# Optimization experiments

Hardware: AMD Instinct MI355X
Metric: run time of the kernel (lower is better)

Reference implementation:

```python
import jax, jax.numpy as jnp
import numpy as np

INPUT_DIM = 512
HIDDEN_DIM = 1024
NUM_LAYERS = 2
B, S = 32, 512


def _xavier(key, shape):
    fan_out, fan_in = shape
    limit = float(np.sqrt(6.0 / (fan_in + fan_out)))
    return jax.random.uniform(key, shape, jnp.float32, -limit, limit)


def setup_inputs() -> dict:
    key = jax.random.key(0)
    ks = jax.random.split(key, 8)
    x = jax.random.normal(ks[0], (B, S, INPUT_DIM), jnp.float32)
    # layer 0: input_dim -> hidden, layer 1: hidden -> hidden
    Wih0 = _xavier(ks[1], (3 * HIDDEN_DIM, INPUT_DIM))
    Whh0 = _xavier(ks[2], (3 * HIDDEN_DIM, HIDDEN_DIM))
    b0 = jnp.zeros((3 * HIDDEN_DIM,), jnp.float32)
    Wih1 = _xavier(ks[3], (3 * HIDDEN_DIM, HIDDEN_DIM))
    Whh1 = _xavier(ks[4], (3 * HIDDEN_DIM, HIDDEN_DIM))
    b1 = jnp.zeros((3 * HIDDEN_DIM,), jnp.float32)
    Wlin = _xavier(ks[5], (INPUT_DIM, HIDDEN_DIM))
    blin = jnp.zeros((INPUT_DIM,), jnp.float32)
    return {"x": x, "Wih0": Wih0, "Whh0": Whh0, "b0": b0,
            "Wih1": Wih1, "Whh1": Whh1, "b1": b1,
            "Wlin": Wlin, "blin": blin}


def _gru_layer(x_tm, h0, Wih, Whh, b):
    # x_tm: [S, B, D_in] time-major; h0: [B, H]
    H = HIDDEN_DIM
    Whn = Whh[2 * H: 3 * H]  # [H, H] used twice per the original cell

    def step(h, x_t):
        gates = x_t @ Wih.T + h @ Whh.T + b          # [B, 3H]
        r, z, n = jnp.split(gates, 3, axis=1)
        r = jax.nn.sigmoid(r)
        z = jax.nn.sigmoid(z)
        # NOTE: original cell adds h@Whn a second time, scaled by r (nonstandard)
        n = jnp.tanh(n + r * (h @ Whn.T))
        h_new = (1.0 - z) * n + z * h
        return h_new, h_new

    h_last, ys = jax.lax.scan(step, h0, x_tm)
    return ys, h_last  # ys: [S, B, H]


def reference(x, Wih0, Whh0, b0, Wih1, Whh1, b1, Wlin, blin):
    # dropout=0.0 -> identity (eval mode)
    x_tm = jnp.swapaxes(x, 0, 1)  # [S, B, D]
    h0 = jnp.zeros((x.shape[0], HIDDEN_DIM), x.dtype)
    y0, h_last0 = _gru_layer(x_tm, h0, Wih0, Whh0, b0)
    y1, h_last1 = _gru_layer(y0, h0, Wih1, Whh1, b1)
    layer_output = jnp.swapaxes(y1, 0, 1)            # [B, S, H]
    out = layer_output @ Wlin.T + blin               # [B, S, INPUT_DIM]
    new_hidden = jnp.stack([h_last0, h_last1], axis=0)  # [L, B, H]
    return out, new_hidden
```

## Files before the change

### kernel.cpp

```cpp
#include <hip/hip_runtime.h>
#include <math.h>

#define B_  32
#define S_  512
#define H_  1024
#define SENT32 0x7F7F7F7Fu

typedef __attribute__((ext_vector_type(8))) short bf16x8;
typedef __attribute__((ext_vector_type(4))) float f32x4;
typedef __attribute__((ext_vector_type(4))) unsigned int u32x4;

__device__ __forceinline__ unsigned short f2bf(float f) {
  unsigned int u = __float_as_uint(f);
  u = (u + 0x7FFFu + ((u >> 16) & 1u)) >> 16;
  return (unsigned short)u;
}

__device__ __forceinline__ void ld4_mall(const unsigned short* p, u32x4& r) {
  asm volatile("global_load_dwordx4 %0, %1, off sc0 sc1" : "=v"(r) : "v"(p));
}
__device__ __forceinline__ void st_mall_b32(unsigned short* p, unsigned int v) {
  asm volatile("global_store_dword %0, %1, off sc0 sc1" :: "v"(p), "v"(v) : "memory");
}

#define BAR_LGKM() do {                                   \
  __builtin_amdgcn_sched_barrier(0);                      \
  asm volatile("s_waitcnt lgkmcnt(0)" ::: "memory");      \
  __builtin_amdgcn_s_barrier();                           \
  __builtin_amdgcn_sched_barrier(0);                      \
} while (0)

__device__ __forceinline__ bf16x8 ld8_f32_to_bf16(const float* p) {
  float4 a = *(const float4*)p;
  float4 b = *(const float4*)(p + 4);
  union { unsigned short s[8]; bf16x8 v; } u;
  u.s[0] = f2bf(a.x); u.s[1] = f2bf(a.y); u.s[2] = f2bf(a.z); u.s[3] = f2bf(a.w);
  u.s[4] = f2bf(b.x); u.s[5] = f2bf(b.y); u.s[6] = f2bf(b.z); u.s[7] = f2bf(b.w);
  return u.v;
}

__global__ void cast_transpose_x(const float* __restrict__ x, unsigned short* __restrict__ xtm) {
  int s = blockIdx.x & 511, b = blockIdx.x >> 9;
  int k = threadIdx.x * 4;
  float4 v = *(const float4*)(x + ((size_t)b * S_ + s) * 512 + k);
  ushort4 o = { f2bf(v.x), f2bf(v.y), f2bf(v.z), f2bf(v.w) };
  *(ushort4*)(xtm + ((size_t)s * B_ + b) * 512 + k) = o;
}


__global__ __launch_bounds__(512, 2)
void gru_fused(const float* __restrict__ wih0, const float* __restrict__ whh0,
               const float* __restrict__ b0,
               const float* __restrict__ wih1, const float* __restrict__ whh1,
               const float* __restrict__ b1,
               const unsigned short* __restrict__ xtm,
               const float* __restrict__ wlin, const float* __restrict__ blin,
               unsigned short* __restrict__ hx0, unsigned short* __restrict__ hx1,
               float* __restrict__ out,
               float* __restrict__ hlast0, float* __restrict__ hlast1) {
  __shared__ __align__(16) float part[8 * 2 * 3 * 64 * 4];
  const int tid  = threadIdx.x;
  const int lane = tid & 63;
  const int w    = tid >> 6;
  const int r16  = lane & 15;
  const int q    = lane >> 4;

  union AU { unsigned int dd[4]; u32x4 u4; bf16x8 v; };

  if (blockIdx.x >= 128) {
    const int nj0 = ((int)blockIdx.x - 128) * 16;
    const int kbase = w * 128;
    const int blkbase = kbase >> 4;
    bf16x8 bwp[4];
#pragma unroll
    for (int c = 0; c < 4; ++c)
      bwp[c] = ld8_f32_to_bf16(wlin + (size_t)(nj0 + r16) * H_ + kbase + c * 32 + q * 8);
    const int eb = tid >> 4, ejj = tid & 15;
    const int em = eb >> 4, eq2 = (eb >> 2) & 3, ereg = eb & 3;
    const float bl = blin[nj0 + ejj];
    const int hxLaneOff = ((q >> 1) * 512) + r16 * 16 + (q & 1) * 8;

    for (int t = 0; t < S_; ++t) {
      const unsigned short* hp = hx1 + ((size_t)t * 64 + blkbase) * 512 + hxLaneOff;
      AU a0[4], a1[4];
      int spins = 0;
      for (;;) {
#pragma unroll
        for (int c = 0; c < 4; ++c) {
          ld4_mall(hp + c * 1024, a0[c].u4);
          ld4_mall(hp + c * 1024 + 256, a1[c].u4);
        }
        asm volatile("s_waitcnt vmcnt(0)"
          : "+v"(a0[0].u4), "+v"(a0[1].u4), "+v"(a0[2].u4), "+v"(a0[3].u4),
            "+v"(a1[0].u4), "+v"(a1[1].u4), "+v"(a1[2].u4), "+v"(a1[3].u4)
          :: "memory");
        __builtin_amdgcn_sched_barrier(0);
        int ok = 1;
#pragma unroll
        for (int c = 0; c < 4; ++c)
#pragma unroll
          for (int d = 0; d < 4; ++d)
            ok &= (a0[c].dd[d] != SENT32) & (a1[c].dd[d] != SENT32);
        if (__all(ok)) break;
        if (++spins > (1 << 16)) break;
        __builtin_amdgcn_s_sleep(32);
      }

      f32x4 acc[2];
#pragma unroll
      for (int m = 0; m < 2; ++m)
#pragma unroll
        for (int u = 0; u < 4; ++u) acc[m][u] = 0.f;
#pragma unroll
      for (int c = 0; c < 4; ++c) {
        acc[0] = __builtin_amdgcn_mfma_f32_16x16x32_bf16(a0[c].v, bwp[c], acc[0], 0, 0, 0);
        acc[1] = __builtin_amdgcn_mfma_f32_16x16x32_bf16(a1[c].v, bwp[c], acc[1], 0, 0, 0);
      }
#pragma unroll
      for (int m = 0; m < 2; ++m)
        *(f32x4*)&part[((w * 2 + m) * 64 + lane) * 4] = acc[m];
      BAR_LGKM();
      {
        float s = 0.f;
#pragma unroll
        for (int ww = 0; ww < 8; ++ww)
          s += part[((ww * 2 + em) * 64 + eq2 * 16 + ejj) * 4 + ereg];
        out[((size_t)eb * S_ + t) * 512 + nj0 + ejj] = s + bl;
      }
      BAR_LGKM();
    }
    return;
  }

  const bool L1  = blockIdx.x >= 64;
  const int  j0  = (L1 ? (int)blockIdx.x - 64 : (int)blockIdx.x) * 16;
  const int  myblk = j0 >> 4;
  const bool hiw = w >= 4;

  const float* Wsrc;
  int wstride, kbase, ncha;
  if (!L1) {
    if (!hiw) { Wsrc = wih0; wstride = 512;  kbase = w * 128;       ncha = 4; }
    else      { Wsrc = whh0; wstride = 1024; kbase = (w - 4) * 256; ncha = 8; }
  } else {
    if (!hiw) { Wsrc = wih1; wstride = 1024; kbase = w * 256;       ncha = 8; }
    else      { Wsrc = whh1; wstride = 1024; kbase = (w - 4) * 256; ncha = 8; }
  }
  const int blkbase = kbase >> 4;

  bf16x8 bw[3][8];
#pragma unroll
  for (int g = 0; g < 3; ++g)
#pragma unroll
    for (int c = 0; c < 8; ++c)
      if (c < ncha)
        bw[g][c] = ld8_f32_to_bf16(Wsrc + (size_t)(g * H_ + j0 + r16) * wstride + kbase + c * 32 + q * 8);

  const int eb  = tid >> 4;
  const int ejj = tid & 15;
  const int em  = eb >> 4, eq2 = (eb >> 2) & 3, ereg = eb & 3;
  const float* bias = L1 ? b1 : b0;
  const float brv = bias[j0 + ejj];
  const float bzv = bias[H_ + j0 + ejj];
  const float bnv = bias[2 * H_ + j0 + ejj];
  float phv = 0.f;

  unsigned short* hxbuf = L1 ? hx1 : hx0;
  float*          hlast = L1 ? hlast1 : hlast0;

  const int hxLaneOff = ((q >> 1) * 512) + r16 * 16 + (q & 1) * 8;

  for (int t = 0; t < S_; ++t) {
    AU a0[8], a1[8];
    if (!hiw && !L1) {
      const unsigned short* ap0 = xtm + (size_t)t * B_ * 512 + (size_t)r16 * 512 + kbase + q * 8;
      const unsigned short* ap1 = ap0 + 16 * 512;
#pragma unroll
      for (int c = 0; c < 8; ++c) if (c < ncha) {
        a0[c].v = *(const bf16x8*)(ap0 + c * 32);
        a1[c].v = *(const bf16x8*)(ap1 + c * 32);
      }
    } else if (hiw && t == 0) {
#pragma unroll
      for (int c = 0; c < 8; ++c)
#pragma unroll
        for (int d = 0; d < 4; ++d) { a0[c].dd[d] = 0u; a1[c].dd[d] = 0u; }
    } else {
      const unsigned short* hp = (!hiw)
        ? hx0   + ((size_t)t * 64 + blkbase) * 512 + hxLaneOff
        : hxbuf + ((size_t)(t - 1) * 64 + blkbase) * 512 + hxLaneOff;
      int spins = 0;
      for (;;) {
#pragma unroll
        for (int c = 0; c < 8; ++c) {
          ld4_mall(hp + c * 1024, a0[c].u4);
          ld4_mall(hp + c * 1024 + 256, a1[c].u4);
        }
        asm volatile("s_waitcnt vmcnt(0)"
          : "+v"(a0[0].u4), "+v"(a0[1].u4), "+v"(a0[2].u4), "+v"(a0[3].u4),
            "+v"(a0[4].u4), "+v"(a0[5].u4), "+v"(a0[6].u4), "+v"(a0[7].u4),
            "+v"(a1[0].u4), "+v"(a1[1].u4), "+v"(a1[2].u4), "+v"(a1[3].u4),
            "+v"(a1[4].u4), "+v"(a1[5].u4), "+v"(a1[6].u4), "+v"(a1[7].u4)
          :: "memory");
        __builtin_amdgcn_sched_barrier(0);
        int ok = 1;
#pragma unroll
        for (int c = 0; c < 8; ++c)
#pragma unroll
          for (int d = 0; d < 4; ++d)
            ok &= (a0[c].dd[d] != SENT32) & (a1[c].dd[d] != SENT32);
        if (__all(ok)) break;
        if (++spins > (1 << 20)) break;
        if (spins > 8) __builtin_amdgcn_s_sleep(1);
      }
    }

    f32x4 acc[2][3];
#pragma unroll
    for (int m = 0; m < 2; ++m)
#pragma unroll
      for (int g = 0; g < 3; ++g)
#pragma unroll
        for (int u = 0; u < 4; ++u) acc[m][g][u] = 0.f;

#pragma unroll
    for (int c = 0; c < 8; ++c) if (c < ncha)
#pragma unroll
      for (int g = 0; g < 3; ++g) {
        acc[0][g] = __builtin_amdgcn_mfma_f32_16x16x32_bf16(a0[c].v, bw[g][c], acc[0][g], 0, 0, 0);
        acc[1][g] = __builtin_amdgcn_mfma_f32_16x16x32_bf16(a1[c].v, bw[g][c], acc[1][g], 0, 0, 0);
      }

#pragma unroll
    for (int m = 0; m < 2; ++m)
#pragma unroll
      for (int g = 0; g < 3; ++g)
        *(f32x4*)&part[(((w * 2 + m) * 3 + g) * 64 + lane) * 4] = acc[m][g];
    BAR_LGKM();

    {
      float hr = 0.f, hz = 0.f, nx = 0.f, nh = 0.f;
#pragma unroll
      for (int ww = 0; ww < 8; ++ww) {
        int base = (ww * 2 + em) * 3;
        float vr = part[((base + 0) * 64 + eq2 * 16 + ejj) * 4 + ereg];
        float vz = part[((base + 1) * 64 + eq2 * 16 + ejj) * 4 + ereg];
        float vn = part[((base + 2) * 64 + eq2 * 16 + ejj) * 4 + ereg];
        hr += vr; hz += vz;
        if (ww < 4) nx += vn; else nh += vn;
      }
      float r  = __builtin_amdgcn_rcpf(1.f + __expf(-(hr + brv)));
      float z  = __builtin_amdgcn_rcpf(1.f + __expf(-(hz + bzv)));
      float a2 = nx + bnv + nh + r * nh;
      float nn = 1.f - 2.f * __builtin_amdgcn_rcpf(__expf(2.f * a2) + 1.f);
      float hv = (1.f - z) * nn + z * phv;
      phv = hv;
      float other = __shfl_xor(hv, 1);
      if ((ejj & 1) == 0) {
        unsigned int pk = (unsigned int)f2bf(hv) | ((unsigned int)f2bf(other) << 16);
        st_mall_b32(hxbuf + ((size_t)t * 64 + myblk) * 512 + eb * 16 + ejj, pk);
        if (t == S_ - 1) {
          hlast[eb * H_ + j0 + ejj]     = hv;
          hlast[eb * H_ + j0 + ejj + 1] = other;
        }
      }
    }
    BAR_LGKM();
  }
}

extern "C" void kernel_launch(void* const* d_in, const int* in_sizes, int n_in,
                              void* d_out, int out_size, void* d_ws, size_t ws_size,
                              hipStream_t stream) {
  const float* x    = (const float*)d_in[0];
  const float* Wih0 = (const float*)d_in[1];
  const float* Whh0 = (const float*)d_in[2];
  const float* b0   = (const float*)d_in[3];
  const float* Wih1 = (const float*)d_in[4];
  const float* Whh1 = (const float*)d_in[5];
  const float* b1   = (const float*)d_in[6];
  const float* Wlin = (const float*)d_in[7];
  const float* blin = (const float*)d_in[8];
  float* out = (float*)d_out;

  char* p = (char*)d_ws;
  size_t off = 0;
  auto alloc = [&](size_t bytes) { void* r = p + off; off += (bytes + 255) & ~(size_t)255; return r; };

  unsigned short* xtm = (unsigned short*)alloc((size_t)8388608 * 2);
  unsigned short* hx0 = (unsigned short*)alloc((size_t)16777216 * 2);
  unsigned short* hx1 = (unsigned short*)alloc((size_t)16777216 * 2);

  (void)hipMemsetAsync(hx0, 0x7F, (size_t)16777216 * 2, stream);
  (void)hipMemsetAsync(hx1, 0x7F, (size_t)16777216 * 2, stream);

  cast_transpose_x<<<16384, 128, 0, stream>>>(x, xtm);

  float* hlast0 = out + 8388608;
  float* hlast1 = out + 8388608 + B_ * H_;

  gru_fused<<<160, 512, 0, stream>>>(Wih0, Whh0, b0, Wih1, Whh1, b1,
                                     xtm, Wlin, blin, hx0, hx1, out,
                                     hlast0, hlast1);
}
```

Before: 1.809 ms.

## Double-buffer GRU partial sums and overlap next-step fetch with gate epilogue

Double-buffers the LDS partial-sum array so the second barrier per timestep can be removed. The elementwise gate epilogue moves onto the first four waves, with each thread handling two hidden units, which also removes the shuffle. The other four waves begin polling for the next step's hidden state right away, after a short sleep. The low waves prefetch the next step's input or layer-0 hidden state once their epilogue is done. This shortens the serial critical path of each recurrent step, at the cost of more register pressure and reliance on the alternating buffers staying race-free.

Measured after the change: 6.232 ms. +244.5%, slower.

```diff
diff --git a/kernel.cpp b/kernel.cpp
--- a/kernel.cpp
+++ b/kernel.cpp
@@ -58,7 +58,7 @@
                unsigned short* __restrict__ hx0, unsigned short* __restrict__ hx1,
                float* __restrict__ out,
                float* __restrict__ hlast0, float* __restrict__ hlast1) {
-  __shared__ __align__(16) float part[8 * 2 * 3 * 64 * 4];
+  __shared__ __align__(16) float part[2][8 * 2 * 3 * 64 * 4];
   const int tid  = threadIdx.x;
   const int lane = tid & 63;
   const int w    = tid >> 6;
@@ -79,6 +79,7 @@
     const int em = eb >> 4, eq2 = (eb >> 2) & 3, ereg = eb & 3;
     const float bl = blin[nj0 + ejj];
     const int hxLaneOff = ((q >> 1) * 512) + r16 * 16 + (q & 1) * 8;
+    float* pb = part[0];
 
     for (int t = 0; t < S_; ++t) {
       const unsigned short* hp = hx1 + ((size_t)t * 64 + blkbase) * 512 + hxLaneOff;
@@ -118,13 +119,13 @@
       }
 #pragma unroll
       for (int m = 0; m < 2; ++m)
-        *(f32x4*)&part[((w * 2 + m) * 64 + lane) * 4] = acc[m];
+        *(f32x4*)&part[0][((w * 2 + m) * 64 + lane) * 4] = acc[m];
       BAR_LGKM();
       {
         float s = 0.f;
 #pragma unroll
         for (int ww = 0; ww < 8; ++ww)
-          s += part[((ww * 2 + em) * 64 + eq2 * 16 + ejj) * 4 + ereg];
+          s += pb[((ww * 2 + em) * 64 + eq2 * 16 + ejj) * 4 + ereg];
         out[((size_t)eb * S_ + t) * 512 + nj0 + ejj] = s + bl;
       }
       BAR_LGKM();
@@ -156,65 +157,75 @@
       if (c < ncha)
         bw[g][c] = ld8_f32_to_bf16(Wsrc + (size_t)(g * H_ + j0 + r16) * wstride + kbase + c * 32 + q * 8);
 
-  const int eb  = tid >> 4;
-  const int ejj = tid & 15;
+  const int eb  = tid >> 3;
+  const int ejp = (tid & 7) * 2;
   const int em  = eb >> 4, eq2 = (eb >> 2) & 3, ereg = eb & 3;
   const float* bias = L1 ? b1 : b0;
-  const float brv = bias[j0 + ejj];
-  const float bzv = bias[H_ + j0 + ejj];
-  const float bnv = bias[2 * H_ + j0 + ejj];
-  float phv = 0.f;
+  float brv[2], bzv[2], bnv[2], phv[2] = {0.f, 0.f};
+  if (tid < 256) {
+#pragma unroll
+    for (int e = 0; e < 2; ++e) {
+      brv[e] = bias[j0 + ejp + e];
+      bzv[e] = bias[H_ + j0 + ejp + e];
+      bnv[e] = bias[2 * H_ + j0 + ejp + e];
+    }
+  }
 
   unsigned short* hxbuf = L1 ? hx1 : hx0;
   float*          hlast = L1 ? hlast1 : hlast0;
 
   const int hxLaneOff = ((q >> 1) * 512) + r16 * 16 + (q & 1) * 8;
 
+  AU a0[8], a1[8];
+
+  auto pollFetch = [&](const unsigned short* hp, bool delayedFirst) {
+    if (delayedFirst) __builtin_amdgcn_s_sleep(16);
+    int spins = 0;
+    for (;;) {
+#pragma unroll
+      for (int c = 0; c < 8; ++c) {
+        ld4_mall(hp + c * 1024, a0[c].u4);
+        ld4_mall(hp + c * 1024 + 256, a1[c].u4);
+      }
+      asm volatile("s_waitcnt vmcnt(0)"
+        : "+v"(a0[0].u4), "+v"(a0[1].u4), "+v"(a0[2].u4), "+v"(a0[3].u4),
+          "+v"(a0[4].u4), "+v"(a0[5].u4), "+v"(a0[6].u4), "+v"(a0[7].u4),
+          "+v"(a1[0].u4), "+v"(a1[1].u4), "+v"(a1[2].u4), "+v"(a1[3].u4),
+          "+v"(a1[4].u4), "+v"(a1[5].u4), "+v"(a1[6].u4), "+v"(a1[7].u4)
+        :: "memory");
+      __builtin_amdgcn_sched_barrier(0);
+      int ok = 1;
+#pragma unroll
+      for (int c = 0; c < 8; ++c)
+#pragma unroll
+        for (int d = 0; d < 4; ++d)
+          ok &= (a0[c].dd[d] != SENT32) & (a1[c].dd[d] != SENT32);
+      if (__all(ok)) break;
+      if (++spins > (1 << 20)) break;
+      if (spins > 8) __builtin_amdgcn_s_sleep(1);
+    }
+  };
+  auto plainX = [&](int t) {
+    const unsigned short* ap0 = xtm + (size_t)t * B_ * 512 + (size_t)r16 * 512 + kbase + q * 8;
+    const unsigned short* ap1 = ap0 + 16 * 512;
+#pragma unroll
+    for (int c = 0; c < 8; ++c) if (c < ncha) {
+      a0[c].v = *(const bf16x8*)(ap0 + c * 32);
+      a1[c].v = *(const bf16x8*)(ap1 + c * 32);
+    }
+  };
+
+  if (!hiw) {
+    if (!L1) plainX(0);
+    else     pollFetch(hx0 + ((size_t)0 * 64 + blkbase) * 512 + hxLaneOff, false);
+  } else {
+#pragma unroll
+    for (int c = 0; c < 8; ++c)
+#pragma unroll
+      for (int d = 0; d < 4; ++d) { a0[c].dd[d] = 0u; a1[c].dd[d] = 0u; }
+  }
+
   for (int t = 0; t < S_; ++t) {
-    AU a0[8], a1[8];
-    if (!hiw && !L1) {
-      const unsigned short* ap0 = xtm + (size_t)t * B_ * 512 + (size_t)r16 * 512 + kbase + q * 8;
-      const unsigned short* ap1 = ap0 + 16 * 512;
-#pragma unroll
-      for (int c = 0; c < 8; ++c) if (c < ncha) {
-        a0[c].v = *(const bf16x8*)(ap0 + c * 32);
-        a1[c].v = *(const bf16x8*)(ap1 + c * 32);
-      }
-    } else if (hiw && t == 0) {
-#pragma unroll
-      for (int c = 0; c < 8; ++c)
-#pragma unroll
-        for (int d = 0; d < 4; ++d) { a0[c].dd[d] = 0u; a1[c].dd[d] = 0u; }
-    } else {
-      const unsigned short* hp = (!hiw)
-        ? hx0   + ((size_t)t * 64 + blkbase) * 512 + hxLaneOff
-        : hxbuf + ((size_t)(t - 1) * 64 + blkbase) * 512 + hxLaneOff;
-      int spins = 0;
-      for (;;) {
-#pragma unroll
-        for (int c = 0; c < 8; ++c) {
-          ld4_mall(hp + c * 1024, a0[c].u4);
-          ld4_mall(hp + c * 1024 + 256, a1[c].u4);
-        }
-        asm volatile("s_waitcnt vmcnt(0)"
-          : "+v"(a0[0].u4), "+v"(a0[1].u4), "+v"(a0[2].u4), "+v"(a0[3].u4),
-            "+v"(a0[4].u4), "+v"(a0[5].u4), "+v"(a0[6].u4), "+v"(a0[7].u4),
-            "+v"(a1[0].u4), "+v"(a1[1].u4), "+v"(a1[2].u4), "+v"(a1[3].u4),
-            "+v"(a1[4].u4), "+v"(a1[5].u4), "+v"(a1[6].u4), "+v"(a1[7].u4)
-          :: "memory");
-        __builtin_amdgcn_sched_barrier(0);
-        int ok = 1;
-#pragma unroll
-        for (int c = 0; c < 8; ++c)
-#pragma unroll
-          for (int d = 0; d < 4; ++d)
-            ok &= (a0[c].dd[d] != SENT32) & (a1[c].dd[d] != SENT32);
-        if (__all(ok)) break;
-        if (++spins > (1 << 20)) break;
-        if (spins > 8) __builtin_amdgcn_s_sleep(1);
-      }
-    }
-
     f32x4 acc[2][3];
 #pragma unroll
     for (int m = 0; m < 2; ++m)
@@ -231,41 +242,50 @@
         acc[1][g] = __builtin_amdgcn_mfma_f32_16x16x32_bf16(a1[c].v, bw[g][c], acc[1][g], 0, 0, 0);
       }
 
+    float* pb = part[t & 1];
 #pragma unroll
     for (int m = 0; m < 2; ++m)
 #pragma unroll
       for (int g = 0; g < 3; ++g)
-        *(f32x4*)&part[(((w * 2 + m) * 3 + g) * 64 + lane) * 4] = acc[m][g];
+        *(f32x4*)&pb[(((w * 2 + m) * 3 + g) * 64 + lane) * 4] = acc[m][g];
     BAR_LGKM();
 
-    {
-      float hr = 0.f, hz = 0.f, nx = 0.f, nh = 0.f;
-#pragma unroll
-      for (int ww = 0; ww < 8; ++ww) {
-        int base = (ww * 2 + em) * 3;
-        float vr = part[((base + 0) * 64 + eq2 * 16 + ejj) * 4 + ereg];
-        float vz = part[((base + 1) * 64 + eq2 * 16 + ejj) * 4 + ereg];
-        float vn = part[((base + 2) * 64 + eq2 * 16 + ejj) * 4 + ereg];
-        hr += vr; hz += vz;
-        if (ww < 4) nx += vn; else nh += vn;
-      }
-      float r  = __builtin_amdgcn_rcpf(1.f + __expf(-(hr + brv)));
-      float z  = __builtin_amdgcn_rcpf(1.f + __expf(-(hz + bzv)));
-      float a2 = nx + bnv + nh + r * nh;
-      float nn = 1.f - 2.f * __builtin_amdgcn_rcpf(__expf(2.f * a2) + 1.f);
-      float hv = (1.f - z) * nn + z * phv;
-      phv = hv;
-      float other = __shfl_xor(hv, 1);
-      if ((ejj & 1) == 0) {
-        unsigned int pk = (unsigned int)f2bf(hv) | ((unsigned int)f2bf(other) << 16);
-        st_mall_b32(hxbuf + ((size_t)t * 64 + myblk) * 512 + eb * 16 + ejj, pk);
-        if (t == S_ - 1) {
-          hlast[eb * H_ + j0 + ejj]     = hv;
-          hlast[eb * H_ + j0 + ejj + 1] = other;
+    if (tid < 256) {
+      float hv2[2];
+#pragma unroll
+      for (int e = 0; e < 2; ++e) {
+        int jj = ejp + e;
+        float hr = 0.f, hz = 0.f, nx = 0.f, nh = 0.f;
+#pragma unroll
+        for (int ww = 0; ww < 8; ++ww) {
+          int base = (ww * 2 + em) * 3;
+          float vr = pb[((base + 0) * 64 + eq2 * 16 + jj) * 4 + ereg];
+          float vz = pb[((base + 1) * 64 + eq2 * 16 + jj) * 4 + ereg];
+          float vn = pb[((base + 2) * 64 + eq2 * 16 + jj) * 4 + ereg];
+          hr += vr; hz += vz;
+          if (ww < 4) nx += vn; else nh += vn;
         }
-      }
-    }
-    BAR_LGKM();
+        float r  = __builtin_amdgcn_rcpf(1.f + __expf(-(hr + brv[e])));
+        float z  = __builtin_amdgcn_rcpf(1.f + __expf(-(hz + bzv[e])));
+        float a2 = nx + bnv[e] + nh + r * nh;
+        float nn = 1.f - 2.f * __builtin_amdgcn_rcpf(__expf(2.f * a2) + 1.f);
+        float hv = (1.f - z) * nn + z * phv[e];
+        phv[e] = hv; hv2[e] = hv;
+      }
+      unsigned int pk = (unsigned int)f2bf(hv2[0]) | ((unsigned int)f2bf(hv2[1]) << 16);
+      st_mall_b32(hxbuf + ((size_t)t * 64 + myblk) * 512 + eb * 16 + ejp, pk);
+      if (t == S_ - 1) {
+        hlast[eb * H_ + j0 + ejp]     = hv2[0];
+        hlast[eb * H_ + j0 + ejp + 1] = hv2[1];
+      }
+      if (t < S_ - 1) {
+        if (!L1) plainX(t + 1);
+        else     pollFetch(hx0 + ((size_t)(t + 1) * 64 + blkbase) * 512 + hxLaneOff, false);
+      }
+    } else {
+      if (t < S_ - 1)
+        pollFetch(hxbuf + ((size_t)t * 64 + blkbase) * 512 + hxLaneOff, true);
+    }
   }
 }
 
```
